# Kernel tuning notes

Measured on AMD Instinct MI355X. Metric: run time of the kernel, lower is better.

## Reference

```python
import jax, jax.numpy as jnp
import numpy as np

N_NODES = 7
N_OPS = 11
HID = 2048
TEMP = 5.0
TANH_C = 2.5
OP_TANH_RED = 2.5


def setup_inputs() -> dict:
    key = jax.random.key(0)
    ks = jax.random.split(key, 9)
    u = lambda k, shape: (jax.random.uniform(k, shape, jnp.float32) - 0.5) * 0.2  # U(-0.1, 0.1) per reset_parameters
    return {
        "emb": u(ks[0], (N_NODES + 1 + N_OPS, HID)),   # node_op_hidden embedding table
        "W_emb_attn": u(ks[1], (HID, HID)),
        "W_hid_attn": u(ks[2], (HID, HID)),
        "W_v_attn": u(ks[3], (1, HID)),
        "W_soft": u(ks[4], (N_OPS, HID)),
        "b_soft": jnp.zeros((N_OPS,), jnp.float32),     # w_soft.bias filled with 0
        "W_ih": u(ks[5], (4 * HID, HID)),               # torch LSTMCell gate order i,f,g,o
        "W_hh": u(ks[6], (4 * HID, HID)),
        "b_ih": u(ks[7], (4 * HID,)),
        "b_hh": u(ks[8], (4 * HID,)),
    }


def _lstm_cell(x, h, c, W_ih, W_hh, b_ih, b_hh):
    # x,h,c: (1, HID)
    gates = x @ W_ih.T + b_ih + h @ W_hh.T + b_hh  # (1, 4H)
    i, f, g, o = jnp.split(gates, 4, axis=-1)
    c2 = jax.nn.sigmoid(f) * c + jax.nn.sigmoid(i) * jnp.tanh(g)
    h2 = jax.nn.sigmoid(o) * jnp.tanh(c2)
    return h2, c2


def reference(emb, W_emb_attn, W_hid_attn, W_v_attn, W_soft, b_soft, W_ih, W_hh, b_ih, b_hh):
    skey = jax.random.key(42)  # sampling stream (torch multinomial is stochastic; fixed key here)
    h = jnp.zeros((1, HID), emb.dtype)
    c = jnp.zeros((1, HID), emb.dtype)
    inp_embed = jnp.zeros((1, HID), emb.dtype)  # static default input for the very first step
    inp_idx = None                              # embedding index fed to subsequent steps
    log_p = jnp.float32(0.0)
    entropy = jnp.float32(0.0)
    prev_nodes, prev_ops = [], []

    for node_idx in range(N_NODES):
        # --- two predecessor-node selections (attention over emb rows 0..node_idx+1) ---
        for i in range(2):
            embed = inp_embed if (node_idx == 0 and i == 0) else emb[inp_idx][None, :]
            h, c = _lstm_cell(embed, h, c, W_ih, W_hh, b_ih, b_hh)
            query = emb[: node_idx + 2]                                  # (k, HID)
            q = jnp.tanh(query @ W_emb_attn.T + h @ W_hid_attn.T)        # (k, HID), h broadcasts
            logits = (q @ W_v_attn.T).reshape(-1)                        # (k,)
            logits = TANH_C * jnp.tanh(logits / TEMP)
            log_probs = jax.nn.log_softmax(logits)
            probs = jnp.exp(log_probs)
            skey, sk = jax.random.split(skey)
            action = jax.random.categorical(sk, logits)
            prev_nodes.append(action)
            log_p = log_p + log_probs[action]
            entropy = entropy - jnp.sum(log_probs * probs)
            inp_idx = action
        # --- two op selections ---
        for i in range(2):
            embed = emb[inp_idx][None, :]
            h, c = _lstm_cell(embed, h, c, W_ih, W_hh, b_ih, b_hh)
            logits = (h @ W_soft.T + b_soft).reshape(-1)                 # (N_OPS,)
            logits = (TANH_C / OP_TANH_RED) * jnp.tanh(logits / TEMP)
            log_probs = jax.nn.log_softmax(logits)
            probs = jnp.exp(log_probs)
            skey, sk = jax.random.split(skey)
            action = jax.random.categorical(sk, logits)
            prev_ops.append(action)
            log_p = log_p + log_probs[action]
            entropy = entropy - jnp.sum(log_probs * probs)
            inp_idx = action + N_NODES + 1

    return jnp.stack(prev_nodes), jnp.stack(prev_ops), log_p, entropy
```

## Files before the change

### kernel.cpp

```cpp
#include <hip/hip_runtime.h>
#include <stdint.h>
#include <string.h>

#define HID 2048

typedef __attribute__((ext_vector_type(8))) unsigned short u16x8;

__device__ __forceinline__ float h2f(unsigned short u){
  _Float16 f; __builtin_memcpy(&f, &u, 2); return (float)f;
}
__device__ __forceinline__ unsigned short f2h(float f){
  _Float16 g = (_Float16)f; unsigned short u; __builtin_memcpy(&u, &g, 2); return u;
}

__device__ __forceinline__ uint32_t rotl32(uint32_t v, int r){ return (v<<r)|(v>>(32-r)); }

__device__ __forceinline__ void tf2x32(uint32_t k0, uint32_t k1, uint32_t x0, uint32_t x1,
                                       uint32_t& o0, uint32_t& o1){
  uint32_t ks2 = k0 ^ k1 ^ 0x1BD11BDAu;
  x0 += k0; x1 += k1;
  x0+=x1; x1=rotl32(x1,13); x1^=x0;
  x0+=x1; x1=rotl32(x1,15); x1^=x0;
  x0+=x1; x1=rotl32(x1,26); x1^=x0;
  x0+=x1; x1=rotl32(x1,6);  x1^=x0;
  x0+=k1; x1+=ks2+1u;
  x0+=x1; x1=rotl32(x1,17); x1^=x0;
  x0+=x1; x1=rotl32(x1,29); x1^=x0;
  x0+=x1; x1=rotl32(x1,16); x1^=x0;
  x0+=x1; x1=rotl32(x1,24); x1^=x0;
  x0+=ks2; x1+=k0+2u;
  x0+=x1; x1=rotl32(x1,13); x1^=x0;
  x0+=x1; x1=rotl32(x1,15); x1^=x0;
  x0+=x1; x1=rotl32(x1,26); x1^=x0;
  x0+=x1; x1=rotl32(x1,6);  x1^=x0;
  x0+=k0; x1+=k1+3u;
  x0+=x1; x1=rotl32(x1,17); x1^=x0;
  x0+=x1; x1=rotl32(x1,29); x1^=x0;
  x0+=x1; x1=rotl32(x1,16); x1^=x0;
  x0+=x1; x1=rotl32(x1,24); x1^=x0;
  x0+=k1; x1+=ks2+4u;
  x0+=x1; x1=rotl32(x1,13); x1^=x0;
  x0+=x1; x1=rotl32(x1,15); x1^=x0;
  x0+=x1; x1=rotl32(x1,26); x1^=x0;
  x0+=x1; x1=rotl32(x1,6);  x1^=x0;
  x0+=ks2; x1+=k0+5u;
  o0=x0; o1=x1;
}

__device__ __forceinline__ float wave_reduce(float v){
  #pragma unroll
  for (int s=32;s;s>>=1) v += __shfl_xor(v, s);
  return v;
}
__device__ __forceinline__ float dot4(float4 a, float4 b){
  return a.x*b.x + a.y*b.y + a.z*b.z + a.w*b.w;
}

__device__ __forceinline__ int sample_wave(float li, int kk, int lane,
                                           uint32_t* key_arr, int sidx, bool write,
                                           float* sc, int* actions, int slot){
  uint32_t k0 = key_arr[2*sidx], k1 = key_arr[2*sidx+1];
  uint32_t n0,n1,s0,s1;
  tf2x32(k0,k1,0u,0u,n0,n1);
  tf2x32(k0,k1,0u,1u,s0,s1);

  float m = li;
  #pragma unroll
  for (int s=32;s;s>>=1) m = fmaxf(m, __shfl_xor(m,s));
  float e = (lane<kk)? expf(li-m) : 0.f;
  float se = wave_reduce(e);
  float lse = logf(se);

  uint32_t y0,y1; tf2x32(s0,s1,0u,(uint32_t)lane,y0,y1);
  uint32_t bits = y0^y1;
  float f = __uint_as_float((bits>>9)|0x3f800000u) - 1.0f;
  float u = fmaxf(f, 1.17549435e-38f);
  float g = -logf(-logf(u));
  float z = (lane<kk)? li+g : -3.0e38f;
  int idx = lane;
  #pragma unroll
  for (int s=32;s;s>>=1){
    float zo = __shfl_xor(z,s); int io = __shfl_xor(idx,s);
    if (zo > z || (zo == z && io < idx)){ z = zo; idx = io; }
  }
  if (write){
    float lact = __shfl(li, idx);
    float lp = li-m-lse;
    float t = (lane<kk)? -lp*expf(lp) : 0.f;
    float ent = wave_reduce(t);
    if (lane==0){
      sc[0] += lact-m-lse;
      sc[1] += ent;
      actions[slot] = idx;
      key_arr[2*(sidx+1)]   = n0;
      key_arr[2*(sidx+1)+1] = n1;
    }
  }
  return idx;
}

__global__ __launch_bounds__(256) void conv_kernel(const float* __restrict__ A,
                                                   const float* __restrict__ B,
                                                   unsigned short* __restrict__ oA,
                                                   unsigned short* __restrict__ oB,
                                                   int nA8, int nTot8){
  int i = blockIdx.x*256 + threadIdx.x;
  if (i >= nTot8) return;
  const float4* src; unsigned short* dst;
  if (i < nA8){ src = (const float4*)A + (size_t)i*2; dst = oA + (size_t)i*8; }
  else { int q = i - nA8; src = (const float4*)B + (size_t)q*2; dst = oB + (size_t)q*8; }
  float4 lo = src[0], hi = src[1];
  u16x8 o;
  o[0]=f2h(lo.x); o[1]=f2h(lo.y); o[2]=f2h(lo.z); o[3]=f2h(lo.w);
  o[4]=f2h(hi.x); o[5]=f2h(hi.y); o[6]=f2h(hi.z); o[7]=f2h(hi.w);
  *(u16x8*)dst = o;
}

__global__ void init_kernel(float* h0, float* c, float* sc, uint32_t* key_arr){
  int tid = blockIdx.x*blockDim.x + threadIdx.x;
  if (tid < HID){ h0[tid]=0.f; c[tid]=0.f; }
  if (tid==0){ sc[0]=0.f; sc[1]=0.f; key_arr[0]=0u; key_arr[1]=42u; }
}

__global__ __launch_bounds__(256) void eproj_kernel(const float* __restrict__ emb,
                                                    const float* __restrict__ Wq,
                                                    float* __restrict__ E){
  int w = (blockIdx.x*256 + threadIdx.x) >> 6;
  int lane = threadIdx.x & 63;
  if (w >= HID) return;
  const float4* W4 = (const float4*)(Wq + (size_t)w*HID);
  float acc[8];
  #pragma unroll
  for (int i=0;i<8;i++) acc[i]=0.f;
  #pragma unroll
  for (int it=0; it<8; ++it){
    float4 wv = W4[it*64 + lane];
    #pragma unroll
    for (int i=0;i<8;i++){
      float4 ev = ((const float4*)(emb + (size_t)i*HID))[it*64+lane];
      acc[i] += dot4(wv, ev);
    }
  }
  #pragma unroll
  for (int i=0;i<8;i++){
    float v = wave_reduce(acc[i]);
    if (lane==0) E[(size_t)i*HID + w] = v;
  }
}

__global__ __launch_bounds__(256) void pproj_kernel(const float* __restrict__ Wih,
                                                    const float* __restrict__ emb,
                                                    const float* __restrict__ bih,
                                                    const float* __restrict__ bhh,
                                                    float* __restrict__ P){
  __shared__ float4 smem[19*128];
  int tid = threadIdx.x, wid = tid>>6, lane = tid&63;
  int jbase = blockIdx.x*8 + wid*2;
  float acc0[19], acc1[19];
  #pragma unroll
  for (int e=0;e<19;e++){ acc0[e]=0.f; acc1[e]=0.f; }
  for (int ch=0; ch<4; ++ch){
    __syncthreads();
    for (int t = tid; t < 19*128; t += 256){
      int row = t>>7, col = t&127;
      smem[t] = ((const float4*)(emb + (size_t)row*HID + ch*512))[col];
    }
    __syncthreads();
    #pragma unroll
    for (int it=0; it<2; ++it){
      float4 w0 = ((const float4*)(Wih + (size_t)jbase*HID     + ch*512))[it*64+lane];
      float4 w1 = ((const float4*)(Wih + (size_t)(jbase+1)*HID + ch*512))[it*64+lane];
      #pragma unroll
      for (int e=0;e<19;e++){
        float4 ev = smem[e*128 + it*64 + lane];
        acc0[e] += dot4(w0, ev);
        acc1[e] += dot4(w1, ev);
      }
    }
  }
  #pragma unroll
  for (int e=0;e<19;e++){ acc0[e]=wave_reduce(acc0[e]); acc1[e]=wave_reduce(acc1[e]); }
  if (lane==0){
    float b0 = bih[jbase]   + bhh[jbase];
    float b1 = bih[jbase+1] + bhh[jbase+1];
    #pragma unroll
    for (int e=0;e<19;e++){
      P[(size_t)e*4*HID + jbase]   = acc0[e] + b0;
      P[(size_t)e*4*HID + jbase+1] = acc1[e] + b1;
    }
    P[(size_t)19*4*HID + jbase]   = b0;
    P[(size_t)19*4*HID + jbase+1] = b1;
  }
}

__global__ __launch_bounds__(512,4) void lstm_fused(const unsigned short* __restrict__ Whh16,
                                                    const float* __restrict__ P,
                                                    const float* __restrict__ hin,
                                                    float* __restrict__ hout,
                                                    float* __restrict__ c,
                                                    const float* __restrict__ a,
                                                    const float* __restrict__ E,
                                                    const float* __restrict__ Wv,
                                                    const float* __restrict__ Wsoft,
                                                    const float* __restrict__ bsoft,
                                                    uint32_t* __restrict__ key_arr,
                                                    float* __restrict__ sc,
                                                    int* __restrict__ actions,
                                                    int mode, int k, int sidx, int slot,
                                                    int xoff, int xconst){
  __shared__ float4 hs4[512];
  __shared__ float red[8][4];
  __shared__ float slog[11];
  __shared__ int sxi;
  int tid = threadIdx.x, wid = tid>>6, lane = tid&63;
  hs4[tid] = ((const float4*)hin)[tid];
  int tl = wid & 3, khalf = wid >> 2;
  int t = blockIdx.x*4 + tl;
  u16x8 wv[4][2];
  #pragma unroll
  for (int g=0; g<4; ++g){
    const u16x8* wr = (const u16x8*)(Whh16 + ((size_t)(g*HID + t))*HID) + khalf*128;
    wv[g][0] = wr[lane];
    wv[g][1] = wr[64 + lane];
  }
  __syncthreads();
  int xi;
  if (mode == 0){
    xi = xconst;
  } else {
    if (mode == 1){
      if (wid < k){
        const float4* E4 = (const float4*)(E + (size_t)wid*HID);
        const float4* a4 = (const float4*)a;
        const float4* v4 = (const float4*)Wv;
        float s = 0.f;
        #pragma unroll
        for (int it=0; it<8; ++it){
          float4 ev = E4[it*64+lane];
          float4 av = a4[it*64+lane];
          float4 w  = v4[it*64+lane];
          s += tanhf(ev.x+av.x)*w.x + tanhf(ev.y+av.y)*w.y
             + tanhf(ev.z+av.z)*w.z + tanhf(ev.w+av.w)*w.w;
        }
        s = wave_reduce(s);
        if (lane==0) slog[wid] = s;
      }
    } else {
      #pragma unroll
      for (int rep=0; rep<2; ++rep){
        int row = wid + rep*8;
        if (row < 11){
          const float4* W4 = (const float4*)(Wsoft + (size_t)row*HID);
          float s = 0.f;
          #pragma unroll
          for (int it=0; it<8; ++it) s += dot4(W4[it*64+lane], hs4[it*64+lane]);
          s = wave_reduce(s);
          if (lane==0) slog[row] = s + bsoft[row];
        }
      }
    }
    __syncthreads();
    if (wid==0){
      int kk = (mode==1) ? k : 11;
      float li = -3.0e38f;
      if (lane < kk){
        float raw = slog[lane];
        li = (mode==1) ? 2.5f*tanhf(raw*0.2f) : tanhf(raw*0.2f);
      }
      int act = sample_wave(li, kk, lane, key_arr, sidx, blockIdx.x==0,
                            sc, actions, slot);
      if (lane==0) sxi = act + xoff;
    }
    __syncthreads();
    xi = sxi;
  }
  float4 hv[2][2];
  #pragma unroll
  for (int it=0; it<2; ++it){
    int idx = khalf*256 + (it*64+lane)*2;
    hv[it][0] = hs4[idx]; hv[it][1] = hs4[idx+1];
  }
  float acc[4] = {0.f,0.f,0.f,0.f};
  #pragma unroll
  for (int g=0; g<4; ++g){
    #pragma unroll
    for (int it=0; it<2; ++it){
      u16x8 w = wv[g][it];
      acc[g] += h2f(w[0])*hv[it][0].x + h2f(w[1])*hv[it][0].y
              + h2f(w[2])*hv[it][0].z + h2f(w[3])*hv[it][0].w
              + h2f(w[4])*hv[it][1].x + h2f(w[5])*hv[it][1].y
              + h2f(w[6])*hv[it][1].z + h2f(w[7])*hv[it][1].w;
    }
  }
  #pragma unroll
  for (int g=0; g<4; ++g){
    float v = wave_reduce(acc[g]);
    if (lane==0) red[wid][g] = v;
  }
  __syncthreads();
  if (tid < 4){
    int t2 = blockIdx.x*4 + tid;
    const float* Pr = P + (size_t)xi*4*HID;
    float gi = red[tid][0]+red[tid+4][0] + Pr[t2];
    float gf = red[tid][1]+red[tid+4][1] + Pr[HID+t2];
    float gg = red[tid][2]+red[tid+4][2] + Pr[2*HID+t2];
    float go = red[tid][3]+red[tid+4][3] + Pr[3*HID+t2];
    float si = 1.f/(1.f+expf(-gi));
    float sf = 1.f/(1.f+expf(-gf));
    float so = 1.f/(1.f+expf(-go));
    float c2 = sf*c[t2] + si*tanhf(gg);
    float h2 = so*tanhf(c2);
    c[t2]=c2; hout[t2]=h2;
  }
}

__global__ __launch_bounds__(256) void hproj_h16_kernel(const unsigned short* __restrict__ Wh16,
                                                        const float* __restrict__ h,
                                                        float* __restrict__ a){
  __shared__ float4 hs4[512];
  int tid = threadIdx.x, wid = tid>>6, lane = tid&63;
  int j = blockIdx.x*4 + wid;
  const u16x8* W8 = (const u16x8*)(Wh16 + (size_t)j*HID);
  u16x8 wv[4];
  #pragma unroll
  for (int it=0; it<4; ++it) wv[it] = W8[it*64+lane];
  hs4[tid] = ((const float4*)h)[tid];
  hs4[tid+256] = ((const float4*)h)[tid+256];
  __syncthreads();
  float acc = 0.f;
  #pragma unroll
  for (int it=0; it<4; ++it){
    int idx = (it*64+lane)*2;
    float4 h0 = hs4[idx], h1 = hs4[idx+1];
    u16x8 w = wv[it];
    acc += h2f(w[0])*h0.x + h2f(w[1])*h0.y + h2f(w[2])*h0.z + h2f(w[3])*h0.w
         + h2f(w[4])*h1.x + h2f(w[5])*h1.y + h2f(w[6])*h1.z + h2f(w[7])*h1.w;
  }
  acc = wave_reduce(acc);
  if (lane==0) a[j] = acc;
}

__global__ __launch_bounds__(512) void finalize_fused(const float* __restrict__ h,
                                                      const float* __restrict__ Wsoft,
                                                      const float* __restrict__ bsoft,
                                                      uint32_t* __restrict__ key_arr,
                                                      float* __restrict__ sc,
                                                      int* __restrict__ actions,
                                                      float* __restrict__ out){
  __shared__ float4 hs4[512];
  __shared__ float slog[11];
  int tid = threadIdx.x, wid = tid>>6, lane = tid&63;
  hs4[tid] = ((const float4*)h)[tid];
  __syncthreads();
  #pragma unroll
  for (int rep=0; rep<2; ++rep){
    int row = wid + rep*8;
    if (row < 11){
      const float4* W4 = (const float4*)(Wsoft + (size_t)row*HID);
      float s = 0.f;
      #pragma unroll
      for (int it=0; it<8; ++it) s += dot4(W4[it*64+lane], hs4[it*64+lane]);
      s = wave_reduce(s);
      if (lane==0) slog[row] = s + bsoft[row];
    }
  }
  __syncthreads();
  if (wid==0){
    float li = (lane<11) ? tanhf(slog[lane]*0.2f) : -3.0e38f;
    int act = sample_wave(li, 11, lane, key_arr, 27, true, sc, actions, 27);
    if (lane==0){
      out[27] = (float)act;
      out[28] = sc[0] + (li - li);
    }
  }
  __syncthreads();
  if (tid==0){ out[28] = sc[0]; out[29] = sc[1]; }
  if (tid < 27) out[tid] = (float)actions[tid];
}

extern "C" void kernel_launch(void* const* d_in, const int* in_sizes, int n_in,
                              void* d_out, int out_size, void* d_ws, size_t ws_size,
                              hipStream_t stream) {
  const float* emb   = (const float*)d_in[0];
  const float* Wq    = (const float*)d_in[1];
  const float* Wh    = (const float*)d_in[2];
  const float* Wv    = (const float*)d_in[3];
  const float* Wsoft = (const float*)d_in[4];
  const float* bsoft = (const float*)d_in[5];
  const float* Wih   = (const float*)d_in[6];
  const float* Whh   = (const float*)d_in[7];
  const float* bih   = (const float*)d_in[8];
  const float* bhh   = (const float*)d_in[9];
  float* out = (float*)d_out;

  const size_t nWhh = (size_t)4*HID*HID;
  const size_t nWh  = (size_t)HID*HID;
  const size_t halfBytes = (nWhh + nWh) * 2;

  unsigned short* Whh16 = (unsigned short*)d_ws;
  unsigned short* Wh16  = Whh16 + nWhh;
  float* fbase = (float*)((char*)d_ws + halfBytes);

  float* h0      = fbase;
  float* h1      = h0 + HID;
  float* c       = h1 + HID;
  float* E       = c  + HID;
  float* P       = E  + 8*HID;
  float* a       = P  + 20*4*HID;
  float* sc      = a + HID;
  uint32_t* key_arr = (uint32_t*)(sc + 2);
  int* actions   = (int*)(key_arr + 58);

  {
    int nA8 = (int)(nWhh/8), nTot8 = (int)((nWhh+nWh)/8);
    conv_kernel<<<(nTot8+255)/256,256,0,stream>>>(Whh, Wh, Whh16, Wh16, nA8, nTot8);
  }
  init_kernel<<<8,256,0,stream>>>(h0, c, sc, key_arr);
  eproj_kernel<<<512,256,0,stream>>>(emb, Wq, E);
  pproj_kernel<<<1024,256,0,stream>>>(Wih, emb, bih, bhh, P);

  float* hbuf[2] = {h0, h1};
  int cur = 0, s = 0;
  for (int node = 0; node < 7; ++node){
    for (int i = 0; i < 4; ++i){
      int mode, kk=0, slot=0, xoff=0;
      if (s == 0){ mode = 0; }
      else {
        int ps = s-1, pi = ps%4, pn = ps/4;
        if (pi < 2){ mode = 1; kk = pn+2; slot = pn*2+pi; xoff = 0; }
        else       { mode = 2; kk = 11;  slot = 14+pn*2+(pi-2); xoff = 8; }
      }
      lstm_fused<<<512,512,0,stream>>>(Whh16, P, hbuf[cur], hbuf[cur^1], c,
                                       a, E, Wv, Wsoft, bsoft,
                                       key_arr, sc, actions,
                                       mode, kk, s-1, slot, xoff, 19);
      cur ^= 1;
      if (i < 2) hproj_h16_kernel<<<512,256,0,stream>>>(Wh16, hbuf[cur], a);
      s++;
    }
  }
  finalize_fused<<<1,512,0,stream>>>(hbuf[cur], Wsoft, bsoft, key_arr, sc, actions, out);
}
```

Baseline: 519.7 us.

## Give LSTM blocks a dedicated sampling wave and full-row gate dot products

The fused LSTM step kernel now runs 256 blocks of 9 waves instead of 512 blocks of 8. Eight waves each compute a full K=2048 row for one hidden unit across the four gates, which removes the split-K shared-memory reduction. The ninth wave computes the attention or softmax logits and samples the action, overlapping that work with the weight dot products and cutting one block-wide barrier. In exchange, logits are computed serially by a single wave, registers per thread double, and fewer blocks are launched.

```diff
diff --git a/kernel.cpp b/kernel.cpp
--- a/kernel.cpp
+++ b/kernel.cpp
@@ -193,7 +193,7 @@
   }
 }
 
-__global__ __launch_bounds__(512,4) void lstm_fused(const unsigned short* __restrict__ Whh16,
+__global__ __launch_bounds__(576,1) void lstm_fused(const unsigned short* __restrict__ Whh16,
                                                     const float* __restrict__ P,
                                                     const float* __restrict__ hin,
                                                     float* __restrict__ hout,
@@ -209,108 +209,88 @@
                                                     int mode, int k, int sidx, int slot,
                                                     int xoff, int xconst){
   __shared__ float4 hs4[512];
-  __shared__ float red[8][4];
-  __shared__ float slog[11];
   __shared__ int sxi;
   int tid = threadIdx.x, wid = tid>>6, lane = tid&63;
-  hs4[tid] = ((const float4*)hin)[tid];
-  int tl = wid & 3, khalf = wid >> 2;
-  int t = blockIdx.x*4 + tl;
-  u16x8 wv[4][2];
-  #pragma unroll
-  for (int g=0; g<4; ++g){
-    const u16x8* wr = (const u16x8*)(Whh16 + ((size_t)(g*HID + t))*HID) + khalf*128;
-    wv[g][0] = wr[lane];
-    wv[g][1] = wr[64 + lane];
-  }
-  __syncthreads();
-  int xi;
-  if (mode == 0){
-    xi = xconst;
-  } else {
-    if (mode == 1){
-      if (wid < k){
-        const float4* E4 = (const float4*)(E + (size_t)wid*HID);
+  if (tid < 512) hs4[tid] = ((const float4*)hin)[tid];
+  int t = blockIdx.x*8 + (wid & 7);
+  u16x8 wv[4][4];
+  if (wid < 8){
+    #pragma unroll
+    for (int g=0; g<4; ++g){
+      const u16x8* wr = (const u16x8*)(Whh16 + ((size_t)(g*HID + t))*HID);
+      #pragma unroll
+      for (int it=0; it<4; ++it) wv[g][it] = wr[it*64 + lane];
+    }
+  }
+  __syncthreads();
+  float acc[4] = {0.f,0.f,0.f,0.f};
+  if (wid == 8){
+    if (mode == 0){
+      if (lane==0) sxi = xconst;
+    } else {
+      int kk = (mode==1) ? k : 11;
+      float li = -3.0e38f;
+      if (mode == 1){
         const float4* a4 = (const float4*)a;
         const float4* v4 = (const float4*)Wv;
-        float s = 0.f;
-        #pragma unroll
-        for (int it=0; it<8; ++it){
-          float4 ev = E4[it*64+lane];
-          float4 av = a4[it*64+lane];
-          float4 w  = v4[it*64+lane];
-          s += tanhf(ev.x+av.x)*w.x + tanhf(ev.y+av.y)*w.y
-             + tanhf(ev.z+av.z)*w.z + tanhf(ev.w+av.w)*w.w;
+        for (int i=0;i<kk;++i){
+          const float4* E4 = (const float4*)(E + (size_t)i*HID);
+          float s = 0.f;
+          #pragma unroll
+          for (int it=0; it<8; ++it){
+            float4 ev = E4[it*64+lane];
+            float4 av = a4[it*64+lane];
+            float4 w  = v4[it*64+lane];
+            s += tanhf(ev.x+av.x)*w.x + tanhf(ev.y+av.y)*w.y
+               + tanhf(ev.z+av.z)*w.z + tanhf(ev.w+av.w)*w.w;
+          }
+          s = wave_reduce(s);
+          if (lane==i) li = 2.5f*tanhf(s*0.2f);
         }
-        s = wave_reduce(s);
-        if (lane==0) slog[wid] = s;
-      }
-    } else {
-      #pragma unroll
-      for (int rep=0; rep<2; ++rep){
-        int row = wid + rep*8;
-        if (row < 11){
-          const float4* W4 = (const float4*)(Wsoft + (size_t)row*HID);
+      } else {
+        for (int i=0;i<11;++i){
+          const float4* W4 = (const float4*)(Wsoft + (size_t)i*HID);
           float s = 0.f;
           #pragma unroll
           for (int it=0; it<8; ++it) s += dot4(W4[it*64+lane], hs4[it*64+lane]);
           s = wave_reduce(s);
-          if (lane==0) slog[row] = s + bsoft[row];
+          if (lane==i) li = tanhf((s + bsoft[i])*0.2f);
         }
       }
-    }
-    __syncthreads();
-    if (wid==0){
-      int kk = (mode==1) ? k : 11;
-      float li = -3.0e38f;
-      if (lane < kk){
-        float raw = slog[lane];
-        li = (mode==1) ? 2.5f*tanhf(raw*0.2f) : tanhf(raw*0.2f);
-      }
+      if (lane >= kk) li = -3.0e38f;
       int act = sample_wave(li, kk, lane, key_arr, sidx, blockIdx.x==0,
                             sc, actions, slot);
       if (lane==0) sxi = act + xoff;
     }
-    __syncthreads();
-    xi = sxi;
-  }
-  float4 hv[2][2];
-  #pragma unroll
-  for (int it=0; it<2; ++it){
-    int idx = khalf*256 + (it*64+lane)*2;
-    hv[it][0] = hs4[idx]; hv[it][1] = hs4[idx+1];
-  }
-  float acc[4] = {0.f,0.f,0.f,0.f};
-  #pragma unroll
-  for (int g=0; g<4; ++g){
-    #pragma unroll
-    for (int it=0; it<2; ++it){
-      u16x8 w = wv[g][it];
-      acc[g] += h2f(w[0])*hv[it][0].x + h2f(w[1])*hv[it][0].y
-              + h2f(w[2])*hv[it][0].z + h2f(w[3])*hv[it][0].w
-              + h2f(w[4])*hv[it][1].x + h2f(w[5])*hv[it][1].y
-              + h2f(w[6])*hv[it][1].z + h2f(w[7])*hv[it][1].w;
-    }
-  }
-  #pragma unroll
-  for (int g=0; g<4; ++g){
-    float v = wave_reduce(acc[g]);
-    if (lane==0) red[wid][g] = v;
-  }
-  __syncthreads();
-  if (tid < 4){
-    int t2 = blockIdx.x*4 + tid;
+  } else {
+    #pragma unroll
+    for (int it=0; it<4; ++it){
+      int idx = (it*64+lane)*2;
+      float4 h0 = hs4[idx], h1 = hs4[idx+1];
+      #pragma unroll
+      for (int g=0; g<4; ++g){
+        u16x8 w = wv[g][it];
+        acc[g] += h2f(w[0])*h0.x + h2f(w[1])*h0.y + h2f(w[2])*h0.z + h2f(w[3])*h0.w
+                + h2f(w[4])*h1.x + h2f(w[5])*h1.y + h2f(w[6])*h1.z + h2f(w[7])*h1.w;
+      }
+    }
+    #pragma unroll
+    for (int g=0; g<4; ++g) acc[g] = wave_reduce(acc[g]);
+  }
+  __syncthreads();
+  if (wid < 8 && lane == 0){
+    int xi = sxi;
     const float* Pr = P + (size_t)xi*4*HID;
-    float gi = red[tid][0]+red[tid+4][0] + Pr[t2];
-    float gf = red[tid][1]+red[tid+4][1] + Pr[HID+t2];
-    float gg = red[tid][2]+red[tid+4][2] + Pr[2*HID+t2];
-    float go = red[tid][3]+red[tid+4][3] + Pr[3*HID+t2];
+    float gi = acc[0] + Pr[t];
+    float gf = acc[1] + Pr[HID+t];
+    float gg = acc[2] + Pr[2*HID+t];
+    float go = acc[3] + Pr[3*HID+t];
     float si = 1.f/(1.f+expf(-gi));
     float sf = 1.f/(1.f+expf(-gf));
     float so = 1.f/(1.f+expf(-go));
-    float c2 = sf*c[t2] + si*tanhf(gg);
+    float c2 = sf*c[t] + si*tanhf(gg);
     float h2 = so*tanhf(c2);
-    c[t2]=c2; hout[t2]=h2;
+    c[t]=c2; hout[t]=h2;
   }
 }
 
@@ -368,10 +348,7 @@
   if (wid==0){
     float li = (lane<11) ? tanhf(slog[lane]*0.2f) : -3.0e38f;
     int act = sample_wave(li, 11, lane, key_arr, 27, true, sc, actions, 27);
-    if (lane==0){
-      out[27] = (float)act;
-      out[28] = sc[0] + (li - li);
-    }
+    if (lane==0) out[27] = (float)act;
   }
   __syncthreads();
   if (tid==0){ out[28] = sc[0]; out[29] = sc[1]; }
@@ -430,7 +407,7 @@
         if (pi < 2){ mode = 1; kk = pn+2; slot = pn*2+pi; xoff = 0; }
         else       { mode = 2; kk = 11;  slot = 14+pn*2+(pi-2); xoff = 8; }
       }
-      lstm_fused<<<512,512,0,stream>>>(Whh16, P, hbuf[cur], hbuf[cur^1], c,
+      lstm_fused<<<256,576,0,stream>>>(Whh16, P, hbuf[cur], hbuf[cur^1], c,
                                        a, E, Wv, Wsoft, bsoft,
                                        key_arr, sc, actions,
                                        mode, kk, s-1, slot, xoff, 19);
```

New measurement: 767.3 us. +47.6%, slower.
